# Optimization experiments

Hardware: AMD Instinct MI355X
Metric: run time of the kernel (lower is better)

Reference implementation:

```python
import jax, jax.numpy as jnp
import numpy as np

EPS = 1e-12

def _l2norm(x):
    return x * jax.lax.rsqrt(jnp.maximum(jnp.sum(x * x, -1, keepdims=True), EPS))

def _reverse_seq(x, lens):
    # per-row reversal of the first `lens[b]` steps (tf.reverse_sequence semantics)
    T = x.shape[1]
    ar = jnp.arange(T)[None, :]
    idx = jnp.where(ar < lens[:, None], lens[:, None] - 1 - ar, ar)
    return jnp.take_along_axis(x, idx[:, :, None], axis=1)

def _lstm(x, lens, Wx, Wh, b):
    # x: [B,T,D]; outputs zeroed past lens, state frozen past lens (dynamic_rnn)
    B, T, _ = x.shape
    H = Wh.shape[0]
    xW = jnp.einsum('btd,dh->bth', x, Wx) + b  # [B,T,4H]
    def step(carry, inp):
        h, c = carry
        xw_t, t = inp
        gates = xw_t + h @ Wh
        i, f, g, o = jnp.split(gates, 4, axis=-1)
        c_new = jax.nn.sigmoid(f) * c + jax.nn.sigmoid(i) * jnp.tanh(g)
        h_new = jax.nn.sigmoid(o) * jnp.tanh(c_new)
        valid = (t < lens)[:, None]
        return (jnp.where(valid, h_new, h), jnp.where(valid, c_new, c)), jnp.where(valid, h_new, 0.0)
    z = jnp.zeros((B, H), x.dtype)
    _, outs = jax.lax.scan(step, (z, z), (xW.transpose(1, 0, 2), jnp.arange(T)))
    return outs.transpose(1, 0, 2)

def _bilstm(x, lens, Wx_f, Wh_f, b_f, Wx_b, Wh_b, b_b):
    fwd = _lstm(x, lens, Wx_f, Wh_f, b_f)
    bwd = _reverse_seq(_lstm(_reverse_seq(x, lens), lens, Wx_b, Wh_b, b_b), lens)
    return jnp.concatenate([fwd, bwd], -1)  # [B,T,2R]

def setup_inputs() -> dict:
    B, T, CTX, D, R, HA, TD = 4096, 80, 10, 300, 200, 100, 256
    V, NTOK, NTY, PL = 100000, 250, 113, 3
    ks = jax.random.split(jax.random.key(0), 16)
    f32 = jnp.float32
    return {
        'input_data': jax.random.randint(ks[0], (B, T), 0, V, jnp.int32),
        'entMentIndex': jax.random.randint(ks[1], (B, 5), 0, B * T, jnp.int32),
        'entCtxLeftIndex': jax.random.randint(ks[2], (B, CTX), 0, B * T, jnp.int32),
        'entCtxRightIndex': jax.random.randint(ks[3], (B, CTX), 0, B * T, jnp.int32),
        'entMentLent': jnp.full((B, 1), 5.0, f32),
        'ctxLeftLent': jnp.full((B, 1), float(CTX), f32),
        'ctxRightLent': jnp.full((B, 1), float(CTX), f32),
        'type_path': jax.random.randint(ks[4], (NTY, PL), 0, NTOK, jnp.int32),
        'word_embed': jax.random.normal(ks[5], (V, D), f32) * 0.1,
        'h_m': jax.random.normal(ks[6], (D, HA), f32) * 0.01,
        'h1': jax.random.normal(ks[7], (2 * R, HA), f32) * 0.01,
        'h2': jax.random.normal(ks[8], (HA, 1), f32) * 0.01,
        'Wx_f': jax.random.normal(ks[9], (D, 4 * R), f32) * 0.05,
        'Wh_f': jax.random.normal(ks[10], (R, 4 * R), f32) * 0.05,
        'b_f': jnp.zeros((4 * R,), f32),
        'Wx_b': jax.random.normal(ks[11], (D, 4 * R), f32) * 0.05,
        'Wh_b': jax.random.normal(ks[12], (R, 4 * R), f32) * 0.05,
        'b_b': jnp.zeros((4 * R,), f32),
        'dense_W': jax.random.normal(ks[13], (D + 2 * R, TD), f32) * 0.05,
        'dense_b': jnp.zeros((TD,), f32),
        'type_tok': jax.random.normal(ks[14], (NTOK, TD), f32) * 0.01,
    }

def reference(input_data, entMentIndex, entCtxLeftIndex, entCtxRightIndex,
              entMentLent, ctxLeftLent, ctxRightLent, type_path, word_embed,
              h_m, h1, h2, Wx_f, Wh_f, b_f, Wx_b, Wh_b, b_b,
              dense_W, dense_b, type_tok):
    D = word_embed.shape[1]
    # flattened sentence embeddings with zero padding row at the end
    flat = jnp.concatenate(
        [jnp.take(word_embed, input_data.reshape(-1), axis=0),
         jnp.zeros((1, D), word_embed.dtype)], 0)
    # mention feature: mean of mention word vectors
    f1 = jnp.take(flat, entMentIndex, axis=0).sum(1) / entMentLent  # [B,D]
    # context features via shared BiLSTM
    left = jnp.take(flat, entCtxLeftIndex, axis=0)
    right = jnp.take(flat, entCtxRightIndex, axis=0)
    f2 = _bilstm(left, ctxLeftLent[:, 0].astype(jnp.int32), Wx_f, Wh_f, b_f, Wx_b, Wh_b, b_b)
    f3 = _bilstm(right, ctxRightLent[:, 0].astype(jnp.int32), Wx_f, Wh_f, b_f, Wx_b, Wh_b, b_b)
    ctx = jnp.concatenate([f2, f3], 1)  # [B, 2*CTX, 2R]
    # attention pooling (non-BBN branch uses relu)
    att = jax.nn.relu(jnp.einsum('btr,rh->bth', ctx, h1) + (f1 @ h_m)[:, None, :])
    w = jax.nn.softmax((att @ h2)[:, :, 0], axis=-1)  # [B, 2*CTX]
    ctx_feat = jnp.einsum('btr,bt->br', ctx, w)
    feat = jnp.concatenate([f1, ctx_feat], 1)  # [B, D+2R]
    ent = _l2norm(jax.nn.relu(feat @ dense_W + dense_b))  # [B, TD]
    # type-path embeddings: sum token embeddings along path, l2-normalize
    type_pad = jnp.concatenate([type_tok, jnp.zeros((1, type_tok.shape[1]), type_tok.dtype)], 0)
    type_norm = _l2norm(jnp.take(type_pad, type_path, axis=0).sum(1))  # [NTY, TD]
    return ent @ type_norm.T  # [B, NTY]
```

## Files before the change

kernel.cpp:

```cpp
#include <hip/hip_runtime.h>
#include <hip/hip_bf16.h>

constexpr int B    = 4096;
constexpr int T    = 80;
constexpr int CTXN = 10;
constexpr int D    = 300;
constexpr int R    = 200;
constexpr int HA   = 100;
constexpr int TD   = 256;
constexpr int NTY  = 113;
constexpr int PL   = 3;
constexpr int NTOK = 250;
constexpr int CTX2 = 20;
constexpr int R2   = 400;
constexpr int FEAT = 700;

constexpr int XSB  = 320;
constexpr int KH   = 256;
constexpr int KW   = 576;
constexpr int NB   = 832;
constexpr int CTXS = 448;
constexpr int DREG = 224;
constexpr int F1S  = 320;
constexpr int FBS  = 704;
constexpr int FMS  = 128;
constexpr int MX   = 2 * B * CTXN;

typedef __attribute__((ext_vector_type(8))) short bf16x8;
typedef __attribute__((ext_vector_type(4))) float f32x4;

__device__ __forceinline__ ushort f2bf(float f) {
    union { float f; uint32_t u; } x{f};
    uint32_t r = x.u + 0x7fff + ((x.u >> 16) & 1);
    return (ushort)(r >> 16);
}
__device__ __forceinline__ float bf2f(ushort u) {
    union { uint32_t u; float f; } x{(uint32_t)u << 16};
    return x.f;
}
__device__ __forceinline__ float fsig(float x) {
    return __builtin_amdgcn_rcpf(1.f + __expf(-x));
}
__device__ __forceinline__ float ftanh(float x) {
    return 1.f - 2.f * __builtin_amdgcn_rcpf(__expf(2.f * x) + 1.f);
}

#define GLD_LDS(g, l) __builtin_amdgcn_global_load_lds( \
    (const __attribute__((address_space(1))) void*)(g), \
    (__attribute__((address_space(3))) void*)(l), 16, 0, 0)
#define GLD_LDS_NT(g, l) __builtin_amdgcn_global_load_lds( \
    (const __attribute__((address_space(1))) void*)(g), \
    (__attribute__((address_space(3))) void*)(l), 16, 0, 2)

constexpr int NWC = 2 * NB * KW;
__global__ void k_prepw3(const float* __restrict__ Wx_f, const float* __restrict__ Wh_f,
                         const float* __restrict__ bf_, const float* __restrict__ Wx_b,
                         const float* __restrict__ Wh_b, const float* __restrict__ bb_,
                         ushort* __restrict__ Wcat, float* __restrict__ biasb) {
    int gid = blockIdx.x * blockDim.x + threadIdx.x;
    if (gid < NWC) {
        int k = gid % KW;
        int q = gid / KW;
        int np = q % NB, dir = q / NB;
        int rb = np >> 6, g = (np >> 4) & 3, ri = np & 15;
        int r = rb * 16 + ri, col = g * 200 + r;
        float v = 0.f;
        if (r < R) {
            if (k < KH) {
                if (k < R) v = (dir ? Wh_b : Wh_f)[(size_t)k * 800 + col];
            } else {
                int kx = k - KH;
                if (kx < D) v = (dir ? Wx_b : Wx_f)[(size_t)kx * 800 + col];
            }
        }
        Wcat[gid] = f2bf(v);
    } else if (gid < NWC + 2 * NB) {
        int t = gid - NWC;
        int np = t % NB, dirb = t / NB;
        int rb = np >> 6, g = (np >> 4) & 3, ri = np & 15;
        int r = rb * 16 + ri, col = g * 200 + r;
        biasb[t] = (r < R) ? (dirb ? bb_ : bf_)[col] : 0.f;
    }
}

__global__ void k_preph1(const float* __restrict__ h1, ushort* __restrict__ h1t) {
    int gid = blockIdx.x * blockDim.x + threadIdx.x;
    if (gid >= FMS * CTXS) return;
    int k = gid % CTXS, n = gid / CTXS;
    float v = 0.f;
    if (n < HA) {
        if (k < DREG) {
            if (k < R) v = h1[(size_t)k * HA + n];
        } else {
            int r2 = k - DREG;
            if (r2 < R) v = h1[(size_t)(R + r2) * HA + n];
        }
    }
    h1t[gid] = f2bf(v);
}
__global__ void k_prephm(const float* __restrict__ h_m, ushort* __restrict__ h_mt) {
    int gid = blockIdx.x * blockDim.x + threadIdx.x;
    if (gid >= FMS * F1S) return;
    int k = gid % F1S, n = gid / F1S;
    float v = (n < HA && k < D) ? h_m[(size_t)k * HA + n] : 0.f;
    h_mt[gid] = f2bf(v);
}
__global__ void k_prepdw(const float* __restrict__ dW, ushort* __restrict__ dWt) {
    int gid = blockIdx.x * blockDim.x + threadIdx.x;
    if (gid >= TD * FBS) return;
    int k = gid % FBS, n = gid / FBS;
    float v = (k < FEAT) ? dW[(size_t)k * TD + n] : 0.f;
    dWt[gid] = f2bf(v);
}

__global__ void k_gatherb(const int* __restrict__ idxL, const int* __restrict__ idxR,
                          const int* __restrict__ input_data,
                          const float* __restrict__ we,
                          ushort* __restrict__ xb) {
    int row = blockIdx.x * 4 + (threadIdx.x >> 6);
    int lane = threadIdx.x & 63;
    if (row >= MX) return;
    int side = row / (B * CTXN);
    int bt = row % (B * CTXN);
    int idx = (side ? idxR : idxL)[bt];
    int w = (idx >= 0 && idx < B * T) ? input_data[idx] : -1;
    ushort* dst = xb + (size_t)row * XSB;
    if (lane < XSB / 8) {
        int e0 = lane * 8;
        ushort tmp[8];
        #pragma unroll
        for (int j = 0; j < 8; ++j) {
            int e = e0 + j;
            float f = (w >= 0 && e < D) ? we[(size_t)w * D + e] : 0.f;
            tmp[j] = f2bf(f);
        }
        *reinterpret_cast<bf16x8*>(dst + e0) = *reinterpret_cast<bf16x8*>(tmp);
    }
}

__global__ void k_f1(const int* __restrict__ ment_idx,
                     const float* __restrict__ ment_lent,
                     const int* __restrict__ input_data,
                     const float* __restrict__ we,
                     ushort* __restrict__ featb, ushort* __restrict__ f1b) {
    int b = blockIdx.x;
    __shared__ int wrow[5];
    if (threadIdx.x < 5) {
        int idx = ment_idx[b * 5 + threadIdx.x];
        wrow[threadIdx.x] = (idx >= 0 && idx < B * T) ? input_data[idx] : -1;
    }
    __syncthreads();
    float inv = 1.0f / ment_lent[b];
    for (int d = threadIdx.x; d < F1S; d += blockDim.x) {
        float s = 0.f;
        if (d < D) {
            #pragma unroll
            for (int j = 0; j < 5; ++j) {
                int w = wrow[j];
                if (w >= 0) s += we[(size_t)w * D + d];
            }
            s *= inv;
        }
        ushort u = f2bf(s);
        if (d < D) featb[(size_t)b * FBS + d] = u;
        f1b[(size_t)b * F1S + d] = u;
    }
}

template<int MODE>
__global__ __launch_bounds__(256) void k_mfma(
    const ushort* __restrict__ A, int lda,
    const ushort* __restrict__ Bt, int ldb,
    float* __restrict__ C, int ldc, int K,
    const float* __restrict__ aux) {
    __shared__ __align__(16) ushort As[128 * 64];
    __shared__ __align__(16) ushort Bs[64 * 64];
    int tid = threadIdx.x, wave = tid >> 6, lane = tid & 63;
    int m0 = blockIdx.y * 128, n0 = blockIdx.x * 64;
    int wr = wave >> 1, wc = wave & 1;
    f32x4 acc[4][2] = {};

    for (int k0 = 0; k0 < K; k0 += 64) {
        #pragma unroll
        for (int p = 0; p < 4; ++p) {
            int chunk = p * 4 + wave;
            int row = chunk * 8 + (lane >> 3);
            int ss = (lane & 7) ^ (row & 7);
            GLD_LDS(A + (size_t)(m0 + row) * lda + k0 + ss * 8, As + chunk * 512);
        }
        #pragma unroll
        for (int p = 0; p < 2; ++p) {
            int chunk = p * 4 + wave;
            int row = chunk * 8 + (lane >> 3);
            int ss = (lane & 7) ^ (row & 7);
            GLD_LDS(Bt + (size_t)(n0 + row) * ldb + k0 + ss * 8, Bs + chunk * 512);
        }
        __syncthreads();
        #pragma unroll
        for (int kk = 0; kk < 2; ++kk) {
            bf16x8 a[4], bf[2];
            #pragma unroll
            for (int m = 0; m < 4; ++m) {
                int r = wr * 64 + m * 16 + (lane & 15);
                int ss = (kk * 4 + (lane >> 4)) ^ (r & 7);
                a[m] = *(const bf16x8*)&As[r * 64 + ss * 8];
            }
            #pragma unroll
            for (int n = 0; n < 2; ++n) {
                int r = wc * 32 + n * 16 + (lane & 15);
                int ss = (kk * 4 + (lane >> 4)) ^ (r & 7);
                bf[n] = *(const bf16x8*)&Bs[r * 64 + ss * 8];
            }
            #pragma unroll
            for (int m = 0; m < 4; ++m)
                #pragma unroll
                for (int n = 0; n < 2; ++n)
                    acc[m][n] = __builtin_amdgcn_mfma_f32_16x16x32_bf16(a[m], bf[n], acc[m][n], 0, 0, 0);
        }
        __syncthreads();
    }
    #pragma unroll
    for (int m = 0; m < 4; ++m) {
        #pragma unroll
        for (int n = 0; n < 2; ++n) {
            int c = n0 + wc * 32 + n * 16 + (lane & 15);
            #pragma unroll
            for (int j = 0; j < 4; ++j) {
                int rr = m0 + wr * 64 + m * 16 + (lane >> 4) * 4 + j;
                float v = acc[m][n][j];
                if (MODE == 1) v = fmaxf(v + aux[c], 0.f);
                C[(size_t)rr * ldc + c] = v;
            }
        }
    }
}

#define WISSUE(KT2, HF2) { \
    ushort* dst = &wS[wave][(2 * (KT2) + (HF2)) % 3][0]; \
    _Pragma("unroll") for (int i = 0; i < 2; ++i) { \
        int p = i * 64 + lane; \
        int nl = p >> 2, c8s = p & 3; \
        int c8 = c8s ^ ((nl >> 1) & 3); \
        GLD_LDS(wb + (size_t)((HF2) * 32 + nl) * KW + (KT2) * 32 + c8 * 8, dst + i * 512); \
    } }

__global__ __launch_bounds__(1024, 1) void k_lstm(
    const ushort* __restrict__ xb,
    const ushort* __restrict__ Wcat,
    const float* __restrict__ biasb,
    const float* __restrict__ lentL, const float* __restrict__ lentR,
    ushort* __restrict__ ctxb) {
    __shared__ __align__(16) ushort hS[64 * 256];
    __shared__ __align__(16) ushort xS[64 * 320];
    __shared__ __align__(16) ushort wS[13][3][1024];
    __shared__ int lenS[64];
    __shared__ int xrowS[CTXN][64];

    const int tid = threadIdx.x, wave = tid >> 6, lane = tid & 63;
    const int bid = blockIdx.x, xcd = bid & 7;
    const int dir = xcd >> 2;
    const int idx = (xcd & 3) * 32 + (bid >> 3);
    const int side = idx >> 6, rg = idx & 63;
    const int b0 = rg * 64;
    const ushort* Wd = Wcat + (size_t)dir * NB * KW;
    const int rl = lane & 15, ch = lane >> 4;
    const bool gw = (wave < 13);
    const ushort* wb = gw ? (Wd + (size_t)wave * 64 * KW) : Wd;

    if (tid < 64) {
        int b = b0 + tid;
        int len = (int)((side ? lentR : lentL)[b]);
        len = min(max(len, 0), CTXN);
        lenS[tid] = len;
        for (int s = 0; s < CTXN; ++s) {
            int tt = dir ? ((s < len) ? (len - 1 - s) : s) : s;
            xrowS[s][tid] = (side * (B * CTXN) + b * CTXN + tt) * XSB;
        }
    }
    {
        uint4 zz{0, 0, 0, 0};
        for (int i = tid; i < 64 * 256 / 8; i += 1024)
            reinterpret_cast<uint4*>(hS)[i] = zz;
    }

    float bias_[4];
    #pragma unroll
    for (int g = 0; g < 4; ++g)
        bias_[g] = gw ? biasb[dir * NB + wave * 64 + g * 16 + rl] : 0.f;
    float cst[16];
    #pragma unroll
    for (int j = 0; j < 16; ++j) cst[j] = 0.f;

    __syncthreads();

    for (int c2 = wave; c2 < 40; c2 += 16) {
        int p = c2 * 64 + lane;
        int row = p / 40, c8s = p - row * 40;
        int c8 = c8s ^ (row & 7);
        GLD_LDS_NT(xb + xrowS[0][row] + c8 * 8, xS + c2 * 512);
    }
    __syncthreads();

    for (int s = 0; s < CTXN; ++s) {
        const int ktstart = (s == 0) ? 8 : 0;
        f32x4 acc[4][4] = {};
        if (gw) {
            WISSUE(ktstart, 0);
            WISSUE(ktstart, 1);
            WISSUE(ktstart + 1, 0);
            bf16x8 af[4];
            for (int kt = ktstart; kt < 18; ++kt) {
                {
                    const ushort* abase; int astr, kof;
                    if (kt < 8) { abase = hS; astr = 256; kof = kt * 4; }
                    else        { abase = xS; astr = 320; kof = (kt - 8) * 4; }
                    #pragma unroll
                    for (int m = 0; m < 4; ++m) {
                        int row = m * 16 + rl;
                        int g = (kof + ch) ^ (row & 7);
                        af[m] = *reinterpret_cast<const bf16x8*>(&abase[row * astr + g * 8]);
                    }
                }
                const int c8r = ch ^ ((rl >> 1) & 3);
                if (kt < 17) { asm volatile("s_waitcnt vmcnt(4)" ::: "memory"); }
                else         { asm volatile("s_waitcnt vmcnt(2)" ::: "memory"); }
                {
                    const ushort* wbuf = &wS[wave][(2 * kt) % 3][0];
                    bf16x8 b0 = *reinterpret_cast<const bf16x8*>(&wbuf[(rl) * 32 + c8r * 8]);
                    bf16x8 b1 = *reinterpret_cast<const bf16x8*>(&wbuf[(16 + rl) * 32 + c8r * 8]);
                    if (kt + 1 < 18) WISSUE(kt + 1, 1);
                    #pragma unroll
                    for (int m = 0; m < 4; ++m) {
                        acc[m][0] = __builtin_amdgcn_mfma_f32_16x16x32_bf16(af[m], b0, acc[m][0], 0, 0, 0);
                        acc[m][1] = __builtin_amdgcn_mfma_f32_16x16x32_bf16(af[m], b1, acc[m][1], 0, 0, 0);
                    }
                }
                if (kt < 17) { asm volatile("s_waitcnt vmcnt(4)" ::: "memory"); }
                else         { asm volatile("s_waitcnt vmcnt(0)" ::: "memory"); }
                {
                    const ushort* wbuf = &wS[wave][(2 * kt + 1) % 3][0];
                    bf16x8 b0 = *reinterpret_cast<const bf16x8*>(&wbuf[(rl) * 32 + c8r * 8]);
                    bf16x8 b1 = *reinterpret_cast<const bf16x8*>(&wbuf[(16 + rl) * 32 + c8r * 8]);
                    if (kt + 2 < 18) WISSUE(kt + 2, 0);
                    #pragma unroll
                    for (int m = 0; m < 4; ++m) {
                        acc[m][2] = __builtin_amdgcn_mfma_f32_16x16x32_bf16(af[m], b0, acc[m][2], 0, 0, 0);
                        acc[m][3] = __builtin_amdgcn_mfma_f32_16x16x32_bf16(af[m], b1, acc[m][3], 0, 0, 0);
                    }
                }
            }
        }
        asm volatile("s_waitcnt lgkmcnt(0)" ::: "memory");
        __builtin_amdgcn_s_barrier();

        if (gw) {
            const int r = wave * 16 + rl;
            #pragma unroll
            for (int m = 0; m < 4; ++m) {
                #pragma unroll
                for (int j = 0; j < 4; ++j) {
                    int row = m * 16 + ch * 4 + j;
                    float gi = acc[m][0][j] + bias_[0];
                    float gf = acc[m][1][j] + bias_[1];
                    float gg = acc[m][2][j] + bias_[2];
                    float go = acc[m][3][j] + bias_[3];
                    float si = fsig(gi), sf = fsig(gf), so = fsig(go);
                    float cn = sf * cst[m * 4 + j] + si * ftanh(gg);
                    float hn = so * ftanh(cn);
                    bool live = (s < lenS[row]);
                    if (live) cst[m * 4 + j] = cn;
                    ushort hv = f2bf(live ? hn : 0.f);
                    wS[wave][0][row * 16 + rl] = hv;
                    if (live && r < R)
                        hS[row * 256 + (((r >> 3) ^ (row & 7)) << 3) + (r & 7)] = hv;
                }
            }
        }
        if (s + 1 < CTXN) {
            for (int c2 = wave; c2 < 40; c2 += 16) {
                int p = c2 * 64 + lane;
                int row = p / 40, c8s = p - row * 40;
                int c8 = c8s ^ (row & 7);
                GLD_LDS_NT(xb + xrowS[s + 1][row] + c8 * 8, xS + c2 * 512);
            }
        }
        asm volatile("s_waitcnt lgkmcnt(0)" ::: "memory");
        __builtin_amdgcn_s_barrier();

        for (int i = tid; i < 64 * 28; i += 1024) {
            int row = i / 28, g = i - row * 28;
            int len = lenS[row];
            int tp = (s < len) ? (dir ? (len - 1 - s) : s) : s;
            bf16x8 v{};
            if (g < 26) {
                int rb2 = g >> 1;
                int off = (g & 1) * 8;
                v = *reinterpret_cast<const bf16x8*>(&wS[rb2][0][row * 16 + off]);
            }
            *reinterpret_cast<bf16x8*>(
                ctxb + ((size_t)(b0 + row) * CTX2 + side * CTXN + tp) * CTXS + dir * DREG + g * 8) = v;
        }
        asm volatile("s_waitcnt vmcnt(0) lgkmcnt(0)" ::: "memory");
        __builtin_amdgcn_s_barrier();
    }
}

__global__ __launch_bounds__(256) void k_attsc(
    const ushort* __restrict__ ctxb, const ushort* __restrict__ h1t,
    const float* __restrict__ fm, const float* __restrict__ h2,
    float* __restrict__ scores) {
    __shared__ __align__(16) ushort As[128 * 64];
    __shared__ __align__(16) ushort Bs[128 * 64];
    __shared__ float sred[128][2];
    __shared__ float h2s[128];
    int tid = threadIdx.x, wave = tid >> 6, lane = tid & 63;
    int m0 = blockIdx.x * 128;
    if (tid < 128) h2s[tid] = (tid < HA) ? h2[tid] : 0.f;
    int wr = wave >> 1, wc = wave & 1;
    f32x4 acc[4][4] = {};

    for (int k0 = 0; k0 < CTXS; k0 += 64) {
        #pragma unroll
        for (int p = 0; p < 4; ++p) {
            int chunk = p * 4 + wave;
            int row = chunk * 8 + (lane >> 3);
            int ss = (lane & 7) ^ (row & 7);
            GLD_LDS(ctxb + (size_t)(m0 + row) * CTXS + k0 + ss * 8, As + chunk * 512);
        }
        #pragma unroll
        for (int p = 0; p < 4; ++p) {
            int chunk = p * 4 + wave;
            int row = chunk * 8 + (lane >> 3);
            int ss = (lane & 7) ^ (row & 7);
            GLD_LDS(h1t + (size_t)row * CTXS + k0 + ss * 8, Bs + chunk * 512);
        }
        __syncthreads();
        #pragma unroll
        for (int kk = 0; kk < 2; ++kk) {
            bf16x8 a[4], bf[4];
            #pragma unroll
            for (int m = 0; m < 4; ++m) {
                int r = wr * 64 + m * 16 + (lane & 15);
                int ss = (kk * 4 + (lane >> 4)) ^ (r & 7);
                a[m] = *(const bf16x8*)&As[r * 64 + ss * 8];
            }
            #pragma unroll
            for (int n = 0; n < 4; ++n) {
                int r = wc * 64 + n * 16 + (lane & 15);
                int ss = (kk * 4 + (lane >> 4)) ^ (r & 7);
                bf[n] = *(const bf16x8*)&Bs[r * 64 + ss * 8];
            }
            #pragma unroll
            for (int m = 0; m < 4; ++m)
                #pragma unroll
                for (int n = 0; n < 4; ++n)
                    acc[m][n] = __builtin_amdgcn_mfma_f32_16x16x32_bf16(a[m], bf[n], acc[m][n], 0, 0, 0);
        }
        __syncthreads();
    }
    #pragma unroll
    for (int m = 0; m < 4; ++m) {
        #pragma unroll
        for (int j = 0; j < 4; ++j) {
            int rl = wr * 64 + m * 16 + (lane >> 4) * 4 + j;
            int brow = (m0 + rl) / CTX2;
            float v = 0.f;
            #pragma unroll
            for (int n = 0; n < 4; ++n) {
                int c = wc * 64 + n * 16 + (lane & 15);
                float a = acc[m][n][j] + fm[(size_t)brow * FMS + c];
                v += fmaxf(a, 0.f) * h2s[c];
            }
            #pragma unroll
            for (int o = 1; o < 16; o <<= 1) v += __shfl_xor(v, o, 64);
            if ((lane & 15) == 0) sred[rl][wc] = v;
        }
    }
    __syncthreads();
    if (tid < 128) scores[m0 + tid] = sred[tid][0] + sred[tid][1];
}

__global__ void k_att2(const float* __restrict__ scores,
                       const ushort* __restrict__ ctxb,
                       ushort* __restrict__ featb) {
    int b = blockIdx.x;
    float sc[CTX2];
    #pragma unroll
    for (int t = 0; t < CTX2; ++t) sc[t] = scores[b * CTX2 + t];
    float mx = -1e30f;
    #pragma unroll
    for (int t = 0; t < CTX2; ++t) mx = fmaxf(mx, sc[t]);
    float w[CTX2], sum = 0.f;
    #pragma unroll
    for (int t = 0; t < CTX2; ++t) { w[t] = __expf(sc[t] - mx); sum += w[t]; }
    float inv = 1.f / sum;
    for (int col = threadIdx.x; col < R2; col += 256) {
        int pos = (col < R) ? col : col + (DREG - R);
        float acc = 0.f;
        #pragma unroll
        for (int t = 0; t < CTX2; ++t)
            acc += w[t] * bf2f(ctxb[((size_t)b * CTX2 + t) * CTXS + pos]);
        featb[(size_t)b * FBS + D + col] = f2bf(acc * inv);
    }
    if (threadIdx.x < FBS - FEAT)
        featb[(size_t)b * FBS + FEAT + threadIdx.x] = 0;
}

__device__ __forceinline__ float blk_sum_256(float v, float* red) {
    #pragma unroll
    for (int o = 32; o > 0; o >>= 1) v += __shfl_down(v, o, 64);
    int lane = threadIdx.x & 63, wid = threadIdx.x >> 6;
    if (lane == 0) red[wid] = v;
    __syncthreads();
    float t = red[0] + red[1] + red[2] + red[3];
    __syncthreads();
    return t;
}

__global__ void k_l2norm(float* __restrict__ x, int ncol) {
    int row = blockIdx.x;
    float* p = x + (size_t)row * ncol;
    __shared__ float red[4];
    float ss = 0.f;
    for (int c = threadIdx.x; c < ncol; c += 256) { float v = p[c]; ss += v * v; }
    float tot = blk_sum_256(ss, red);
    float scale = 1.f / sqrtf(fmaxf(tot, 1e-12f));
    for (int c = threadIdx.x; c < ncol; c += 256) p[c] *= scale;
}

__global__ void k_typenorm(const int* __restrict__ type_path,
                           const float* __restrict__ type_tok,
                           float* __restrict__ tnorm) {
    int y = blockIdx.x;
    int c = threadIdx.x;
    __shared__ float red[4];
    float s = 0.f;
    #pragma unroll
    for (int j = 0; j < PL; ++j) {
        int tk = type_path[y * PL + j];
        if (tk >= 0 && tk < NTOK) s += type_tok[(size_t)tk * TD + c];
    }
    float tot = blk_sum_256(s * s, red);
    float scale = 1.f / sqrtf(fmaxf(tot, 1e-12f));
    tnorm[(size_t)y * TD + c] = s * scale;
}

__global__ void k_final(const float* __restrict__ ent,
                        const float* __restrict__ tnorm,
                        float* __restrict__ out) {
    int b = blockIdx.x;
    __shared__ float es[TD];
    for (int c = threadIdx.x; c < TD; c += blockDim.x) es[c] = ent[(size_t)b * TD + c];
    __syncthreads();
    for (int y = threadIdx.x; y < NTY; y += blockDim.x) {
        const float* tn = tnorm + (size_t)y * TD;
        float acc = 0.f;
        #pragma unroll 4
        for (int k = 0; k < TD; ++k) acc += es[k] * tn[k];
        out[(size_t)b * NTY + y] = acc;
    }
}

static inline char* wsalloc(char*& p, size_t bytes) {
    char* r = p;
    p += (bytes + 255) & ~(size_t)255;
    return r;
}

extern "C" void kernel_launch(void* const* d_in, const int* in_sizes, int n_in,
                              void* d_out, int out_size, void* d_ws, size_t ws_size,
                              hipStream_t stream) {
    const int*   input_data       = (const int*)d_in[0];
    const int*   entMentIndex     = (const int*)d_in[1];
    const int*   entCtxLeftIndex  = (const int*)d_in[2];
    const int*   entCtxRightIndex = (const int*)d_in[3];
    const float* entMentLent      = (const float*)d_in[4];
    const float* ctxLeftLent      = (const float*)d_in[5];
    const float* ctxRightLent     = (const float*)d_in[6];
    const int*   type_path        = (const int*)d_in[7];
    const float* word_embed       = (const float*)d_in[8];
    const float* h_m              = (const float*)d_in[9];
    const float* h1               = (const float*)d_in[10];
    const float* h2               = (const float*)d_in[11];
    const float* Wx_f             = (const float*)d_in[12];
    const float* Wh_f             = (const float*)d_in[13];
    const float* b_f              = (const float*)d_in[14];
    const float* Wx_b             = (const float*)d_in[15];
    const float* Wh_b             = (const float*)d_in[16];
    const float* b_b              = (const float*)d_in[17];
    const float* dense_W          = (const float*)d_in[18];
    const float* dense_b          = (const float*)d_in[19];
    const float* type_tok         = (const float*)d_in[20];
    float* out = (float*)d_out;

    char* p = (char*)d_ws;
    ushort* xb    = (ushort*)wsalloc(p, (size_t)MX * XSB * 2);
    ushort* ctxb  = (ushort*)wsalloc(p, (size_t)B * CTX2 * CTXS * 2);
    ushort* featb = (ushort*)wsalloc(p, (size_t)B * FBS * 2);
    ushort* f1b   = (ushort*)wsalloc(p, (size_t)B * F1S * 2);
    float*  fm    = (float*) wsalloc(p, (size_t)B * FMS * 4);
    float*  scores= (float*) wsalloc(p, (size_t)MX * 4);
    float*  ent   = (float*) wsalloc(p, (size_t)B * TD * 4);
    float*  tnorm = (float*) wsalloc(p, (size_t)NTY * TD * 4);
    ushort* Wcat  = (ushort*)wsalloc(p, (size_t)2 * NB * KW * 2);
    float*  biasb = (float*) wsalloc(p, (size_t)2 * NB * 4);
    ushort* h1t   = (ushort*)wsalloc(p, (size_t)FMS * CTXS * 2);
    ushort* h_mt  = (ushort*)wsalloc(p, (size_t)FMS * F1S * 2);
    ushort* dWt   = (ushort*)wsalloc(p, (size_t)TD * FBS * 2);

    {
        int tot = NWC + 2 * NB;
        k_prepw3<<<(tot + 255) / 256, 256, 0, stream>>>(Wx_f, Wh_f, b_f, Wx_b, Wh_b, b_b,
                                                        Wcat, biasb);
    }
    k_preph1<<<(FMS * CTXS + 255) / 256, 256, 0, stream>>>(h1, h1t);
    k_prephm<<<(FMS * F1S + 255) / 256, 256, 0, stream>>>(h_m, h_mt);
    k_prepdw<<<(TD * FBS + 255) / 256, 256, 0, stream>>>(dense_W, dWt);

    k_gatherb<<<(MX + 3) / 4, 256, 0, stream>>>(entCtxLeftIndex, entCtxRightIndex,
                                                input_data, word_embed, xb);
    k_f1<<<B, 256, 0, stream>>>(entMentIndex, entMentLent, input_data, word_embed, featb, f1b);

    k_mfma<3><<<dim3(FMS / 64, B / 128), 256, 0, stream>>>(f1b, F1S, h_mt, F1S, fm, FMS, F1S, nullptr);

    k_lstm<<<256, 1024, 0, stream>>>(xb, Wcat, biasb, ctxLeftLent, ctxRightLent, ctxb);

    k_attsc<<<MX / 128, 256, 0, stream>>>(ctxb, h1t, fm, h2, scores);
    k_att2<<<B, 256, 0, stream>>>(scores, ctxb, featb);

    k_mfma<1><<<dim3(TD / 64, B / 128), 256, 0, stream>>>(featb, FBS, dWt, FBS,
                                                          ent, TD, FBS, dense_b);
    k_l2norm<<<B, 256, 0, stream>>>(ent, TD);
    k_typenorm<<<NTY, TD, 0, stream>>>(type_path, type_tok, tnorm);
    k_final<<<B, 128, 0, stream>>>(ent, tnorm, out);
}
```

Measured before the change: 542.4 us.

## Split LSTM blocks to 32 rows with 8 waves covering two gate blocks

The recurrent LSTM kernel moves from 256 blocks of 1024 threads handling 64 batch rows to 512 blocks of 512 threads handling 32 rows. Each of the 8 waves now computes one or two 64-column gate blocks in sequence, instead of 13 active waves and 3 idle ones. The weight stream changes from a 3-slot ring to a 2-slot double buffer, and the gate math moves ahead of the barrier. The aim is to remove idle waves, raise block count and use LDS more efficiently. The cost is that each 32-row block re-streams the full weights from cache, and each wave runs its gate blocks serially with a shallower prefetch.

```diff
diff --git a/kernel.cpp b/kernel.cpp
--- a/kernel.cpp
+++ b/kernel.cpp
@@ -25,6 +25,7 @@
 constexpr int FBS  = 704;
 constexpr int FMS  = 128;
 constexpr int MX   = 2 * B * CTXN;
+constexpr int MB   = 32;
 
 typedef __attribute__((ext_vector_type(8))) short bf16x8;
 typedef __attribute__((ext_vector_type(4))) float f32x4;
@@ -235,8 +236,8 @@
     }
 }
 
-#define WISSUE(KT2, HF2) { \
-    ushort* dst = &wS[wave][(2 * (KT2) + (HF2)) % 3][0]; \
+#define WISSUE2(KT2, HF2, BUF2) { \
+    ushort* dst = &wS[wave][BUF2][0]; \
     _Pragma("unroll") for (int i = 0; i < 2; ++i) { \
         int p = i * 64 + lane; \
         int nl = p >> 2, c8s = p & 3; \
@@ -244,30 +245,28 @@
         GLD_LDS(wb + (size_t)((HF2) * 32 + nl) * KW + (KT2) * 32 + c8 * 8, dst + i * 512); \
     } }
 
-__global__ __launch_bounds__(1024, 1) void k_lstm(
+__global__ __launch_bounds__(512, 1) void k_lstm(
     const ushort* __restrict__ xb,
     const ushort* __restrict__ Wcat,
     const float* __restrict__ biasb,
     const float* __restrict__ lentL, const float* __restrict__ lentR,
     ushort* __restrict__ ctxb) {
-    __shared__ __align__(16) ushort hS[64 * 256];
-    __shared__ __align__(16) ushort xS[64 * 320];
-    __shared__ __align__(16) ushort wS[13][3][1024];
-    __shared__ int lenS[64];
-    __shared__ int xrowS[CTXN][64];
+    __shared__ __align__(16) ushort hS[MB * 256];
+    __shared__ __align__(16) ushort xS[MB * 320];
+    __shared__ __align__(16) ushort wS[8][2][1024];
+    __shared__ int lenS[MB];
+    __shared__ int xrowS[CTXN][MB];
 
     const int tid = threadIdx.x, wave = tid >> 6, lane = tid & 63;
     const int bid = blockIdx.x, xcd = bid & 7;
     const int dir = xcd >> 2;
-    const int idx = (xcd & 3) * 32 + (bid >> 3);
-    const int side = idx >> 6, rg = idx & 63;
-    const int b0 = rg * 64;
+    const int idx = (xcd & 3) * 64 + (bid >> 3);
+    const int side = idx >> 7, rg = idx & 127;
+    const int b0 = rg * MB;
     const ushort* Wd = Wcat + (size_t)dir * NB * KW;
     const int rl = lane & 15, ch = lane >> 4;
-    const bool gw = (wave < 13);
-    const ushort* wb = gw ? (Wd + (size_t)wave * 64 * KW) : Wd;
-
-    if (tid < 64) {
+
+    if (tid < MB) {
         int b = b0 + tid;
         int len = (int)((side ? lentR : lentL)[b]);
         len = min(max(len, 0), CTXN);
@@ -279,21 +278,26 @@
     }
     {
         uint4 zz{0, 0, 0, 0};
-        for (int i = tid; i < 64 * 256 / 8; i += 1024)
+        for (int i = tid; i < MB * 256 / 8; i += 512)
             reinterpret_cast<uint4*>(hS)[i] = zz;
     }
 
-    float bias_[4];
-    #pragma unroll
-    for (int g = 0; g < 4; ++g)
-        bias_[g] = gw ? biasb[dir * NB + wave * 64 + g * 16 + rl] : 0.f;
-    float cst[16];
-    #pragma unroll
-    for (int j = 0; j < 16; ++j) cst[j] = 0.f;
+    const int nrb = (wave + 8 < 13) ? 2 : 1;
+    float bias_[2][4];
+    #pragma unroll
+    for (int g = 0; g < 4; ++g) {
+        bias_[0][g] = biasb[dir * NB + wave * 64 + g * 16 + rl];
+        bias_[1][g] = (nrb > 1) ? biasb[dir * NB + (wave + 8) * 64 + g * 16 + rl] : 0.f;
+    }
+    float cst[2][8];
+    #pragma unroll
+    for (int i = 0; i < 2; ++i)
+        #pragma unroll
+        for (int j = 0; j < 8; ++j) cst[i][j] = 0.f;
 
     __syncthreads();
 
-    for (int c2 = wave; c2 < 40; c2 += 16) {
+    for (int c2 = wave; c2 < 20; c2 += 8) {
         int p = c2 * 64 + lane;
         int row = p / 40, c8s = p - row * 40;
         int c8 = c8s ^ (row & 7);
@@ -301,83 +305,100 @@
     }
     __syncthreads();
 
+    float hnew[2][8];
+
     for (int s = 0; s < CTXN; ++s) {
         const int ktstart = (s == 0) ? 8 : 0;
-        f32x4 acc[4][4] = {};
-        if (gw) {
-            WISSUE(ktstart, 0);
-            WISSUE(ktstart, 1);
-            WISSUE(ktstart + 1, 0);
-            bf16x8 af[4];
-            for (int kt = ktstart; kt < 18; ++kt) {
-                {
-                    const ushort* abase; int astr, kof;
-                    if (kt < 8) { abase = hS; astr = 256; kof = kt * 4; }
-                    else        { abase = xS; astr = 320; kof = (kt - 8) * 4; }
-                    #pragma unroll
-                    for (int m = 0; m < 4; ++m) {
-                        int row = m * 16 + rl;
-                        int g = (kof + ch) ^ (row & 7);
-                        af[m] = *reinterpret_cast<const bf16x8*>(&abase[row * astr + g * 8]);
+        #pragma unroll
+        for (int rbi = 0; rbi < 2; ++rbi) {
+            if (rbi < nrb) {
+                const int rb = rbi ? (wave + 8) : wave;
+                const ushort* wb = Wd + (size_t)rb * 64 * KW;
+                f32x4 acc[2][4] = {};
+                WISSUE2(ktstart, 0, 0);
+                WISSUE2(ktstart, 1, 1);
+                const int c8r = ch ^ ((rl >> 1) & 3);
+                for (int kt = ktstart; kt < 18; ++kt) {
+                    bf16x8 af[2];
+                    {
+                        const ushort* abase; int astr, kof;
+                        if (kt < 8) { abase = hS; astr = 256; kof = kt * 4; }
+                        else        { abase = xS; astr = 320; kof = (kt - 8) * 4; }
+                        #pragma unroll
+                        for (int m = 0; m < 2; ++m) {
+                            int row = m * 16 + rl;
+                            int g = (kof + ch) ^ (row & 7);
+                            af[m] = *reinterpret_cast<const bf16x8*>(&abase[row * astr + g * 8]);
+                        }
+                    }
+                    asm volatile("s_waitcnt vmcnt(2)" ::: "memory");
+                    {
+                        const ushort* wbuf = &wS[wave][0][0];
+                        bf16x8 b0 = *reinterpret_cast<const bf16x8*>(&wbuf[(rl) * 32 + c8r * 8]);
+                        bf16x8 b1 = *reinterpret_cast<const bf16x8*>(&wbuf[(16 + rl) * 32 + c8r * 8]);
+                        #pragma unroll
+                        for (int m = 0; m < 2; ++m) {
+                            acc[m][0] = __builtin_amdgcn_mfma_f32_16x16x32_bf16(af[m], b0, acc[m][0], 0, 0, 0);
+                            acc[m][1] = __builtin_amdgcn_mfma_f32_16x16x32_bf16(af[m], b1, acc[m][1], 0, 0, 0);
+                        }
+                        if (kt + 1 < 18) WISSUE2(kt + 1, 0, 0);
+                    }
+                    if (kt + 1 < 18) { asm volatile("s_waitcnt vmcnt(2)" ::: "memory"); }
+                    else             { asm volatile("s_waitcnt vmcnt(0)" ::: "memory"); }
+                    {
+                        const ushort* wbuf = &wS[wave][1][0];
+                        bf16x8 b0 = *reinterpret_cast<const bf16x8*>(&wbuf[(rl) * 32 + c8r * 8]);
+                        bf16x8 b1 = *reinterpret_cast<const bf16x8*>(&wbuf[(16 + rl) * 32 + c8r * 8]);
+                        #pragma unroll
+                        for (int m = 0; m < 2; ++m) {
+                            acc[m][2] = __builtin_amdgcn_mfma_f32_16x16x32_bf16(af[m], b0, acc[m][2], 0, 0, 0);
+                            acc[m][3] = __builtin_amdgcn_mfma_f32_16x16x32_bf16(af[m], b1, acc[m][3], 0, 0, 0);
+                        }
+                        if (kt + 1 < 18) WISSUE2(kt + 1, 1, 1);
                     }
                 }
-                const int c8r = ch ^ ((rl >> 1) & 3);
-                if (kt < 17) { asm volatile("s_waitcnt vmcnt(4)" ::: "memory"); }
-                else         { asm volatile("s_waitcnt vmcnt(2)" ::: "memory"); }
-                {
-                    const ushort* wbuf = &wS[wave][(2 * kt) % 3][0];
-                    bf16x8 b0 = *reinterpret_cast<const bf16x8*>(&wbuf[(rl) * 32 + c8r * 8]);
-                    bf16x8 b1 = *reinterpret_cast<const bf16x8*>(&wbuf[(16 + rl) * 32 + c8r * 8]);
-                    if (kt + 1 < 18) WISSUE(kt + 1, 1);
+                #pragma unroll
+                for (int m = 0; m < 2; ++m) {
                     #pragma unroll
-                    for (int m = 0; m < 4; ++m) {
-                        acc[m][0] = __builtin_amdgcn_mfma_f32_16x16x32_bf16(af[m], b0, acc[m][0], 0, 0, 0);
-                        acc[m][1] = __builtin_amdgcn_mfma_f32_16x16x32_bf16(af[m], b1, acc[m][1], 0, 0, 0);
+                    for (int j = 0; j < 4; ++j) {
+                        int row = m * 16 + ch * 4 + j;
+                        float gi = acc[m][0][j] + bias_[rbi][0];
+                        float gf = acc[m][1][j] + bias_[rbi][1];
+                        float gg = acc[m][2][j] + bias_[rbi][2];
+                        float go = acc[m][3][j] + bias_[rbi][3];
+                        float si = fsig(gi), sf = fsig(gf), so = fsig(go);
+                        float cn = sf * cst[rbi][m * 4 + j] + si * ftanh(gg);
+                        float hn = so * ftanh(cn);
+                        if (s < lenS[row]) cst[rbi][m * 4 + j] = cn;
+                        hnew[rbi][m * 4 + j] = hn;
                     }
                 }
-                if (kt < 17) { asm volatile("s_waitcnt vmcnt(4)" ::: "memory"); }
-                else         { asm volatile("s_waitcnt vmcnt(0)" ::: "memory"); }
-                {
-                    const ushort* wbuf = &wS[wave][(2 * kt + 1) % 3][0];
-                    bf16x8 b0 = *reinterpret_cast<const bf16x8*>(&wbuf[(rl) * 32 + c8r * 8]);
-                    bf16x8 b1 = *reinterpret_cast<const bf16x8*>(&wbuf[(16 + rl) * 32 + c8r * 8]);
-                    if (kt + 2 < 18) WISSUE(kt + 2, 0);
+            }
+        }
+        asm volatile("s_waitcnt lgkmcnt(0)" ::: "memory");
+        __builtin_amdgcn_s_barrier();
+
+        #pragma unroll
+        for (int rbi = 0; rbi < 2; ++rbi) {
+            if (rbi < nrb) {
+                const int rb = wave + rbi * 8;
+                const int r = rb * 16 + rl;
+                #pragma unroll
+                for (int m = 0; m < 2; ++m) {
                     #pragma unroll
-                    for (int m = 0; m < 4; ++m) {
-                        acc[m][2] = __builtin_amdgcn_mfma_f32_16x16x32_bf16(af[m], b0, acc[m][2], 0, 0, 0);
-                        acc[m][3] = __builtin_amdgcn_mfma_f32_16x16x32_bf16(af[m], b1, acc[m][3], 0, 0, 0);
+                    for (int j = 0; j < 4; ++j) {
+                        int row = m * 16 + ch * 4 + j;
+                        bool live = (s < lenS[row]);
+                        ushort hv = f2bf(live ? hnew[rbi][m * 4 + j] : 0.f);
+                        wS[wave][1][row * 32 + rbi * 16 + rl] = hv;
+                        if (live && r < R)
+                            hS[row * 256 + (((r >> 3) ^ (row & 7)) << 3) + (r & 7)] = hv;
                     }
                 }
             }
         }
-        asm volatile("s_waitcnt lgkmcnt(0)" ::: "memory");
-        __builtin_amdgcn_s_barrier();
-
-        if (gw) {
-            const int r = wave * 16 + rl;
-            #pragma unroll
-            for (int m = 0; m < 4; ++m) {
-                #pragma unroll
-                for (int j = 0; j < 4; ++j) {
-                    int row = m * 16 + ch * 4 + j;
-                    float gi = acc[m][0][j] + bias_[0];
-                    float gf = acc[m][1][j] + bias_[1];
-                    float gg = acc[m][2][j] + bias_[2];
-                    float go = acc[m][3][j] + bias_[3];
-                    float si = fsig(gi), sf = fsig(gf), so = fsig(go);
-                    float cn = sf * cst[m * 4 + j] + si * ftanh(gg);
-                    float hn = so * ftanh(cn);
-                    bool live = (s < lenS[row]);
-                    if (live) cst[m * 4 + j] = cn;
-                    ushort hv = f2bf(live ? hn : 0.f);
-                    wS[wave][0][row * 16 + rl] = hv;
-                    if (live && r < R)
-                        hS[row * 256 + (((r >> 3) ^ (row & 7)) << 3) + (r & 7)] = hv;
-                }
-            }
-        }
         if (s + 1 < CTXN) {
-            for (int c2 = wave; c2 < 40; c2 += 16) {
+            for (int c2 = wave; c2 < 20; c2 += 8) {
                 int p = c2 * 64 + lane;
                 int row = p / 40, c8s = p - row * 40;
                 int c8 = c8s ^ (row & 7);
@@ -387,15 +408,16 @@
         asm volatile("s_waitcnt lgkmcnt(0)" ::: "memory");
         __builtin_amdgcn_s_barrier();
 
-        for (int i = tid; i < 64 * 28; i += 1024) {
+        for (int i = tid; i < MB * 28; i += 512) {
             int row = i / 28, g = i - row * 28;
             int len = lenS[row];
             int tp = (s < len) ? (dir ? (len - 1 - s) : s) : s;
             bf16x8 v{};
             if (g < 26) {
                 int rb2 = g >> 1;
+                int w = rb2 & 7, rbi = rb2 >> 3;
                 int off = (g & 1) * 8;
-                v = *reinterpret_cast<const bf16x8*>(&wS[rb2][0][row * 16 + off]);
+                v = *reinterpret_cast<const bf16x8*>(&wS[w][1][row * 32 + rbi * 16 + off]);
             }
             *reinterpret_cast<bf16x8*>(
                 ctxb + ((size_t)(b0 + row) * CTX2 + side * CTXN + tp) * CTXS + dir * DREG + g * 8) = v;
@@ -623,7 +645,7 @@
 
     k_mfma<3><<<dim3(FMS / 64, B / 128), 256, 0, stream>>>(f1b, F1S, h_mt, F1S, fm, FMS, F1S, nullptr);
 
-    k_lstm<<<256, 1024, 0, stream>>>(xb, Wcat, biasb, ctxLeftLent, ctxRightLent, ctxb);
+    k_lstm<<<512, 512, 0, stream>>>(xb, Wcat, biasb, ctxLeftLent, ctxRightLent, ctxb);
 
     k_attsc<<<MX / 128, 256, 0, stream>>>(ctxb, h1t, fm, h2, scores);
     k_att2<<<B, 256, 0, stream>>>(scores, ctxb, featb);
```

New measurement: 561.7 us. 3.6% more time.
